# Kernel optimization log

Hardware: AMD Instinct MI355X
Metric: run time of the kernel (lower is better)

## Reference

```python
import jax, jax.numpy as jnp
import numpy as np

NO_TRANS = -10000.0
B, S, T = 512, 1024, 64
START, STOP = 1, 2


def setup_inputs() -> dict:
    key = jax.random.key(0)
    k1, k2, k3, k4 = jax.random.split(key, 4)
    feats = jax.random.normal(k1, (B, S, T), dtype=jnp.float32)
    tags = jax.random.randint(k2, (B, S), 3, T)  # avoid pad/start/stop tags
    lengths = jax.random.randint(k3, (B,), 1, S + 1)
    masks = (jnp.arange(S)[None, :] < lengths[:, None]).astype(jnp.float32)
    transitions = jax.random.normal(k4, (T, T), dtype=jnp.float32) * 0.1
    # replicate the constrained init from __init__ (transitions[next, prev])
    transitions = (transitions
                   .at[START, :].set(NO_TRANS)   # nothing transitions into START
                   .at[:, STOP].set(NO_TRANS)    # nothing transitions out of STOP
                   .at[:, 0].set(NO_TRANS)
                   .at[0, :].set(NO_TRANS))
    return {"feats": feats, "tags": tags, "lengths": lengths, "masks": masks,
            "transitions": transitions, "start_idx": START, "stop_idx": STOP}


def reference(feats, tags, lengths, masks, transitions, start_idx, stop_idx):
    """CRF negative log-likelihood per sequence: log Z (forward algorithm) - gold path score.
    feats: [B,S,T] emissions, transitions: [T,T] (next, prev)."""
    Bsz, Slen, Tsz = feats.shape

    # ---- forward algorithm (log-partition), batched lax.scan over time ----
    init = jnp.full((Bsz, Tsz), NO_TRANS, dtype=feats.dtype).at[:, start_idx].set(0.0)

    def step(fv, emit):  # fv: [B,T] (prev alphas), emit: [B,T]
        # next_tag_var[b, next, prev] = fv[b, prev] + trans[next, prev] + emit[b, next]
        nv = jax.scipy.special.logsumexp(
            fv[:, None, :] + transitions[None, :, :] + emit[:, :, None], axis=2)
        return nv, nv

    _, all_fv = jax.lax.scan(step, init, jnp.swapaxes(feats, 0, 1))  # [S,B,T]
    # pick forward var at the last valid position of each sequence
    fv_final = all_fv[lengths - 1, jnp.arange(Bsz)]                  # [B,T]
    alpha = jax.scipy.special.logsumexp(fv_final + transitions[stop_idx][None, :], axis=1)

    # ---- gold path score (vectorized _score_sentence_batch) ----
    tags_ext = jnp.concatenate(
        [jnp.full((Bsz, 1), start_idx, dtype=tags.dtype), tags], axis=1)  # [B,S+1]
    tn, tc = tags_ext[:, 1:], tags_ext[:, :-1]                            # [B,S]
    trans_sc = transitions[tn, tc] * masks                                # [B,S]
    emit_sc = jnp.take_along_axis(feats, tn[:, :, None], axis=2)[..., 0] * masks
    ends = jnp.take_along_axis(tags_ext, lengths[:, None], axis=1)[:, 0]  # tag at last valid step
    gold = trans_sc.sum(axis=1) + emit_sc.sum(axis=1) + transitions[stop_idx, ends]

    return alpha - gold  # per-sequence NLL, shape [B]
```

## Files before the change

### kernel.cpp

```cpp
#include <hip/hip_runtime.h>


#define TT 64

#define BAR() asm volatile("s_waitcnt lgkmcnt(0)\n\ts_barrier" ::: "memory")

__global__ __launch_bounds__(256, 2) void crf_fwd_kernel(
    const float* __restrict__ feats, const int* __restrict__ tags,
    const int* __restrict__ lengths, const float* __restrict__ trans,
    const int* __restrict__ p_start, const int* __restrict__ p_stop,
    float* __restrict__ out, int B, int S) {
  const int tid = threadIdx.x;
  const int lane = tid & 63;
  const int w = tid >> 6;
  const int cg = lane >> 4;
  const int li = lane & 15;
  const int r = w * 16 + li;
  const int b = blockIdx.x;

  __shared__ float s_trans[TT * TT];
  __shared__ __align__(16) float s_E[2][TT];
  __shared__ float s_part[4];

  for (int i = tid * 4; i < TT * TT; i += 256 * 4) {
    *reinterpret_cast<float4*>(&s_trans[i]) =
        *reinterpret_cast<const float4*>(trans + i);
  }
  __syncthreads();

  const int start = *p_start;
  const int stop = *p_stop;
  const int len = lengths[b];

  float q0, q1, q2, q3, q4, q5, q6, q7, q8, q9, q10, q11, q12, q13, q14, q15;
  {
    const float* wr = s_trans + r * TT + cg * 16;
    float4 t0 = *reinterpret_cast<const float4*>(wr + 0);
    float4 t1 = *reinterpret_cast<const float4*>(wr + 4);
    float4 t2 = *reinterpret_cast<const float4*>(wr + 8);
    float4 t3 = *reinterpret_cast<const float4*>(wr + 12);
    q0 = __expf(t0.x); q1 = __expf(t0.y); q2 = __expf(t0.z); q3 = __expf(t0.w);
    q4 = __expf(t1.x); q5 = __expf(t1.y); q6 = __expf(t1.z); q7 = __expf(t1.w);
    q8 = __expf(t2.x); q9 = __expf(t2.y); q10 = __expf(t2.z); q11 = __expf(t2.w);
    q12 = __expf(t3.x); q13 = __expf(t3.y); q14 = __expf(t3.z); q15 = __expf(t3.w);
  }
  float ws_e = __expf(s_trans[stop * TT + lane]);

  const float* fbase = feats + (size_t)b * S * TT;
  const float* fbr = fbase + r;
  const int* tb = tags + (size_t)b * S;

  {
    float iv = __expf(fbase[r]) * __expf(s_trans[r * TT + start]);
    if (cg == 0) s_E[0][r] = iv;
  }
  int C = 0;
  int buf = 0;
  __syncthreads();

#define PRIME(J)                                                               \
  float e##J = __expf(fbr[(size_t)TT * ((1 + (J)) < S ? (1 + (J)) : S - 1)]);  \
  float f##J = fbr[(size_t)TT * ((9 + (J)) < S ? (9 + (J)) : S - 1)];
  PRIME(0) PRIME(1) PRIME(2) PRIME(3)
  PRIME(4) PRIME(5) PRIME(6) PRIME(7)
#undef PRIME

#define MATVEC16(SUM, XB)                                                      \
  float4 x0 = *reinterpret_cast<const float4*>((XB) + cg * 16 + 0);            \
  float4 x1 = *reinterpret_cast<const float4*>((XB) + cg * 16 + 4);            \
  float4 x2 = *reinterpret_cast<const float4*>((XB) + cg * 16 + 8);            \
  float4 x3 = *reinterpret_cast<const float4*>((XB) + cg * 16 + 12);           \
  float a0 = q0 * x0.x; float a1 = q1 * x0.y;                                  \
  float a2 = q2 * x0.z; float a3 = q3 * x0.w;                                  \
  a0 = fmaf(q4, x1.x, a0); a1 = fmaf(q5, x1.y, a1);                            \
  a2 = fmaf(q6, x1.z, a2); a3 = fmaf(q7, x1.w, a3);                            \
  a0 = fmaf(q8, x2.x, a0); a1 = fmaf(q9, x2.y, a1);                            \
  a2 = fmaf(q10, x2.z, a2); a3 = fmaf(q11, x2.w, a3);                          \
  a0 = fmaf(q12, x3.x, a0); a1 = fmaf(q13, x3.y, a1);                          \
  a2 = fmaf(q14, x3.z, a2); a3 = fmaf(q15, x3.w, a3);                          \
  float SUM = (a0 + a1) + (a2 + a3);                                           \
  SUM += __shfl_xor(SUM, 16, 64);                                              \
  SUM += __shfl_xor(SUM, 32, 64);

#define STEP(J, SBASE, RN)                                                     \
  {                                                                            \
    float ecur = e##J;                                                         \
    e##J = __expf(f##J);                                                       \
    int pidx = (SBASE) + (J) + 16;                                             \
    pidx = pidx < S ? pidx : S - 1;                                             \
    f##J = fbr[(size_t)TT * pidx];                                             \
    const float* Eb = s_E[buf];                                                \
    MATVEC16(sum, Eb);                                                         \
    float En;                                                                  \
    if (RN) {                                                                  \
      unsigned rb = __builtin_bit_cast(unsigned, Eb[3]);                       \
      int k = (int)((rb >> 23) & 0xFFu) - 127;                                 \
      C += k;                                                                  \
      float sc = __builtin_bit_cast(float, (unsigned)(127 - k) << 23);         \
      En = ecur * sum * sc;                                                    \
    } else {                                                                   \
      En = ecur * sum;                                                         \
    }                                                                          \
    if (cg == 0) s_E[buf ^ 1][r] = En;                                         \
    buf ^= 1;                                                                  \
    BAR();                                                                     \
  }

  int s = 1;
#pragma unroll 1
  for (; s + 8 <= len; s += 8) {
    STEP(0, s, 0) STEP(1, s, 0) STEP(2, s, 0) STEP(3, s, 1)
    STEP(4, s, 0) STEP(5, s, 0) STEP(6, s, 0) STEP(7, s, 1)
  }
#pragma unroll 1
  for (; s < len; ++s) {
    const float* Eb = s_E[buf];
    MATVEC16(sum, Eb);
    unsigned rb = __builtin_bit_cast(unsigned, Eb[3]);
    int k = (int)((rb >> 23) & 0xFFu) - 127;
    C += k;
    float sc = __builtin_bit_cast(float, (unsigned)(127 - k) << 23);
    float ecur = __expf(fbr[(size_t)TT * s]);
    float En = ecur * sum * sc;
    if (cg == 0) s_E[buf ^ 1][r] = En;
    buf ^= 1;
    BAR();
  }

  float v = s_E[buf][lane] * ws_e;
#pragma unroll
  for (int off = 32; off >= 1; off >>= 1) v += __shfl_xor(v, off, 64);
  float alpha = __logf(v) + (float)C * 0.6931471805599453f;

  float gs = 0.0f;
#pragma unroll 1
  for (int s0 = 0; s0 < len; s0 += 256) {
    int si = s0 + tid;
    if (si < len) {
      int t = tb[si];
      int tp = (si == 0) ? start : tb[si - 1];
      gs += s_trans[t * TT + tp] + fbase[(size_t)si * TT + t];
    }
  }
#pragma unroll
  for (int off = 32; off >= 1; off >>= 1) gs += __shfl_xor(gs, off, 64);
  if (lane == 0) s_part[w] = gs;
  __syncthreads();
  if (tid == 0) {
    float gold = (s_part[0] + s_part[1]) + (s_part[2] + s_part[3]) +
                 s_trans[stop * TT + tb[len - 1]];
    out[b] = alpha - gold;
  }
}

extern "C" void kernel_launch(void* const* d_in, const int* in_sizes, int n_in,
                              void* d_out, int out_size, void* d_ws, size_t ws_size,
                              hipStream_t stream) {
  const float* feats = (const float*)d_in[0];
  const int* tags = (const int*)d_in[1];
  const int* lengths = (const int*)d_in[2];
  const float* trans = (const float*)d_in[4];
  const int* p_start = (const int*)d_in[5];
  const int* p_stop = (const int*)d_in[6];
  float* out = (float*)d_out;

  int B = in_sizes[2];
  int S = in_sizes[1] / B;
  crf_fwd_kernel<<<B, 256, 0, stream>>>(feats, tags, lengths, trans,
                                        p_start, p_stop, out, B, S);
}
```

Before: 402.3 us.

## Halve block to two waves with 32-wide per-lane matvec and permlane32 reduction

The block shrinks from 4 waves to 2, and each lane now holds 32 exp-transition weights instead of 16. The cross-lane reduction becomes a single permlane32_swap instead of two xor shuffles. The per-step barrier now syncs only two waves, and the matvec loads are issued before the exp/prefetch work. The trade-off is double the FMA and LDS reads per lane on the serial critical path, higher register pressure, and fewer waves to hide latency.

```diff
diff --git a/kernel.cpp b/kernel.cpp
--- a/kernel.cpp
+++ b/kernel.cpp
@@ -3,9 +3,14 @@
 
 #define TT 64
 
-#define BAR() asm volatile("s_waitcnt lgkmcnt(0)\n\ts_barrier" ::: "memory")
+__device__ __forceinline__ float xhalf_sum(float s) {
+  unsigned u = __builtin_bit_cast(unsigned, s);
+  auto p = __builtin_amdgcn_permlane32_swap(u, u, false, false);
+  return __builtin_bit_cast(float, (unsigned)p[0]) +
+         __builtin_bit_cast(float, (unsigned)p[1]);
+}
 
-__global__ __launch_bounds__(256, 2) void crf_fwd_kernel(
+__global__ __launch_bounds__(128, 1) void crf_fwd_kernel(
     const float* __restrict__ feats, const int* __restrict__ tags,
     const int* __restrict__ lengths, const float* __restrict__ trans,
     const int* __restrict__ p_start, const int* __restrict__ p_stop,
@@ -13,16 +18,16 @@
   const int tid = threadIdx.x;
   const int lane = tid & 63;
   const int w = tid >> 6;
-  const int cg = lane >> 4;
-  const int li = lane & 15;
-  const int r = w * 16 + li;
+  const int cg = lane >> 5;
+  const int li = lane & 31;
+  const int r = w * 32 + li;
   const int b = blockIdx.x;
 
   __shared__ float s_trans[TT * TT];
   __shared__ __align__(16) float s_E[2][TT];
-  __shared__ float s_part[4];
+  __shared__ float s_part[2];
 
-  for (int i = tid * 4; i < TT * TT; i += 256 * 4) {
+  for (int i = tid * 4; i < TT * TT; i += 128 * 4) {
     *reinterpret_cast<float4*>(&s_trans[i]) =
         *reinterpret_cast<const float4*>(trans + i);
   }
@@ -32,17 +37,28 @@
   const int stop = *p_stop;
   const int len = lengths[b];
 
-  float q0, q1, q2, q3, q4, q5, q6, q7, q8, q9, q10, q11, q12, q13, q14, q15;
+  float q0, q1, q2, q3, q4, q5, q6, q7, q8, q9, q10, q11, q12, q13, q14, q15,
+      q16, q17, q18, q19, q20, q21, q22, q23, q24, q25, q26, q27, q28, q29,
+      q30, q31;
   {
-    const float* wr = s_trans + r * TT + cg * 16;
-    float4 t0 = *reinterpret_cast<const float4*>(wr + 0);
-    float4 t1 = *reinterpret_cast<const float4*>(wr + 4);
-    float4 t2 = *reinterpret_cast<const float4*>(wr + 8);
-    float4 t3 = *reinterpret_cast<const float4*>(wr + 12);
-    q0 = __expf(t0.x); q1 = __expf(t0.y); q2 = __expf(t0.z); q3 = __expf(t0.w);
-    q4 = __expf(t1.x); q5 = __expf(t1.y); q6 = __expf(t1.z); q7 = __expf(t1.w);
-    q8 = __expf(t2.x); q9 = __expf(t2.y); q10 = __expf(t2.z); q11 = __expf(t2.w);
-    q12 = __expf(t3.x); q13 = __expf(t3.y); q14 = __expf(t3.z); q15 = __expf(t3.w);
+    const float* wr = s_trans + r * TT + (cg << 5);
+    float4 t;
+    t = *reinterpret_cast<const float4*>(wr + 0);
+    q0 = __expf(t.x); q1 = __expf(t.y); q2 = __expf(t.z); q3 = __expf(t.w);
+    t = *reinterpret_cast<const float4*>(wr + 4);
+    q4 = __expf(t.x); q5 = __expf(t.y); q6 = __expf(t.z); q7 = __expf(t.w);
+    t = *reinterpret_cast<const float4*>(wr + 8);
+    q8 = __expf(t.x); q9 = __expf(t.y); q10 = __expf(t.z); q11 = __expf(t.w);
+    t = *reinterpret_cast<const float4*>(wr + 12);
+    q12 = __expf(t.x); q13 = __expf(t.y); q14 = __expf(t.z); q15 = __expf(t.w);
+    t = *reinterpret_cast<const float4*>(wr + 16);
+    q16 = __expf(t.x); q17 = __expf(t.y); q18 = __expf(t.z); q19 = __expf(t.w);
+    t = *reinterpret_cast<const float4*>(wr + 20);
+    q20 = __expf(t.x); q21 = __expf(t.y); q22 = __expf(t.z); q23 = __expf(t.w);
+    t = *reinterpret_cast<const float4*>(wr + 24);
+    q24 = __expf(t.x); q25 = __expf(t.y); q26 = __expf(t.z); q27 = __expf(t.w);
+    t = *reinterpret_cast<const float4*>(wr + 28);
+    q28 = __expf(t.x); q29 = __expf(t.y); q30 = __expf(t.z); q31 = __expf(t.w);
   }
   float ws_e = __expf(s_trans[stop * TT + lane]);
 
@@ -65,32 +81,42 @@
   PRIME(4) PRIME(5) PRIME(6) PRIME(7)
 #undef PRIME
 
-#define MATVEC16(SUM, XB)                                                      \
-  float4 x0 = *reinterpret_cast<const float4*>((XB) + cg * 16 + 0);            \
-  float4 x1 = *reinterpret_cast<const float4*>((XB) + cg * 16 + 4);            \
-  float4 x2 = *reinterpret_cast<const float4*>((XB) + cg * 16 + 8);            \
-  float4 x3 = *reinterpret_cast<const float4*>((XB) + cg * 16 + 12);           \
-  float a0 = q0 * x0.x; float a1 = q1 * x0.y;                                  \
-  float a2 = q2 * x0.z; float a3 = q3 * x0.w;                                  \
+#define MATVEC32(SUM, XB)                                                      \
+  const float* xb = (XB) + (cg << 5);                                          \
+  float4 x0 = *reinterpret_cast<const float4*>(xb + 0);                        \
+  float4 x1 = *reinterpret_cast<const float4*>(xb + 4);                        \
+  float4 x2 = *reinterpret_cast<const float4*>(xb + 8);                        \
+  float4 x3 = *reinterpret_cast<const float4*>(xb + 12);                       \
+  float4 x4 = *reinterpret_cast<const float4*>(xb + 16);                       \
+  float4 x5 = *reinterpret_cast<const float4*>(xb + 20);                       \
+  float4 x6 = *reinterpret_cast<const float4*>(xb + 24);                       \
+  float4 x7 = *reinterpret_cast<const float4*>(xb + 28);                       \
+  float a0 = q0 * x0.x, a1 = q1 * x0.y, a2 = q2 * x0.z, a3 = q3 * x0.w;        \
   a0 = fmaf(q4, x1.x, a0); a1 = fmaf(q5, x1.y, a1);                            \
   a2 = fmaf(q6, x1.z, a2); a3 = fmaf(q7, x1.w, a3);                            \
   a0 = fmaf(q8, x2.x, a0); a1 = fmaf(q9, x2.y, a1);                            \
   a2 = fmaf(q10, x2.z, a2); a3 = fmaf(q11, x2.w, a3);                          \
   a0 = fmaf(q12, x3.x, a0); a1 = fmaf(q13, x3.y, a1);                          \
   a2 = fmaf(q14, x3.z, a2); a3 = fmaf(q15, x3.w, a3);                          \
-  float SUM = (a0 + a1) + (a2 + a3);                                           \
-  SUM += __shfl_xor(SUM, 16, 64);                                              \
-  SUM += __shfl_xor(SUM, 32, 64);
+  a0 = fmaf(q16, x4.x, a0); a1 = fmaf(q17, x4.y, a1);                          \
+  a2 = fmaf(q18, x4.z, a2); a3 = fmaf(q19, x4.w, a3);                          \
+  a0 = fmaf(q20, x5.x, a0); a1 = fmaf(q21, x5.y, a1);                          \
+  a2 = fmaf(q22, x5.z, a2); a3 = fmaf(q23, x5.w, a3);                          \
+  a0 = fmaf(q24, x6.x, a0); a1 = fmaf(q25, x6.y, a1);                          \
+  a2 = fmaf(q26, x6.z, a2); a3 = fmaf(q27, x6.w, a3);                          \
+  a0 = fmaf(q28, x7.x, a0); a1 = fmaf(q29, x7.y, a1);                          \
+  a2 = fmaf(q30, x7.z, a2); a3 = fmaf(q31, x7.w, a3);                          \
+  float SUM = xhalf_sum((a0 + a1) + (a2 + a3));
 
 #define STEP(J, SBASE, RN)                                                     \
   {                                                                            \
+    const float* Eb = s_E[buf];                                                \
+    MATVEC32(sum, Eb);                                                         \
     float ecur = e##J;                                                         \
     e##J = __expf(f##J);                                                       \
     int pidx = (SBASE) + (J) + 16;                                             \
-    pidx = pidx < S ? pidx : S - 1;                                             \
+    pidx = pidx < S ? pidx : S - 1;                                            \
     f##J = fbr[(size_t)TT * pidx];                                             \
-    const float* Eb = s_E[buf];                                                \
-    MATVEC16(sum, Eb);                                                         \
     float En;                                                                  \
     if (RN) {                                                                  \
       unsigned rb = __builtin_bit_cast(unsigned, Eb[3]);                       \
@@ -103,7 +129,7 @@
     }                                                                          \
     if (cg == 0) s_E[buf ^ 1][r] = En;                                         \
     buf ^= 1;                                                                  \
-    BAR();                                                                     \
+    __syncthreads();                                                           \
   }
 
   int s = 1;
@@ -115,7 +141,7 @@
 #pragma unroll 1
   for (; s < len; ++s) {
     const float* Eb = s_E[buf];
-    MATVEC16(sum, Eb);
+    MATVEC32(sum, Eb);
     unsigned rb = __builtin_bit_cast(unsigned, Eb[3]);
     int k = (int)((rb >> 23) & 0xFFu) - 127;
     C += k;
@@ -124,7 +150,7 @@
     float En = ecur * sum * sc;
     if (cg == 0) s_E[buf ^ 1][r] = En;
     buf ^= 1;
-    BAR();
+    __syncthreads();
   }
 
   float v = s_E[buf][lane] * ws_e;
@@ -134,7 +160,7 @@
 
   float gs = 0.0f;
 #pragma unroll 1
-  for (int s0 = 0; s0 < len; s0 += 256) {
+  for (int s0 = 0; s0 < len; s0 += 128) {
     int si = s0 + tid;
     if (si < len) {
       int t = tb[si];
@@ -147,8 +173,7 @@
   if (lane == 0) s_part[w] = gs;
   __syncthreads();
   if (tid == 0) {
-    float gold = (s_part[0] + s_part[1]) + (s_part[2] + s_part[3]) +
-                 s_trans[stop * TT + tb[len - 1]];
+    float gold = s_part[0] + s_part[1] + s_trans[stop * TT + tb[len - 1]];
     out[b] = alpha - gold;
   }
 }
@@ -166,6 +191,6 @@
 
   int B = in_sizes[2];
   int S = in_sizes[1] / B;
-  crf_fwd_kernel<<<B, 256, 0, stream>>>(feats, tags, lengths, trans,
+  crf_fwd_kernel<<<B, 128, 0, stream>>>(feats, tags, lengths, trans,
                                         p_start, p_stop, out, B, S);
 }
```

Measured after the change: 377.4 us. 6.2% less time.
